# Kernel tuning notes

Measured on AMD Instinct MI355X. Metric: run time of the kernel, lower is better.

## Reference

```python
import jax, jax.numpy as jnp
import numpy as np

N = 100000
E = 1600000
IN_C, HID_C, OUT_C = 128, 128, 64


def setup_inputs() -> dict:
    key = jax.random.key(0)
    ks = jax.random.split(key, 8)
    x = jax.random.normal(ks[0], (N, IN_C), dtype=jnp.float32)
    edge_index = jax.random.randint(ks[1], (2, E), 0, N, dtype=jnp.int64)
    # Glorot-ish init for the 3 GCNConv linear weights + zero biases (PyG default)
    def glorot(k, fan_in, fan_out):
        s = jnp.sqrt(6.0 / (fan_in + fan_out))
        return jax.random.uniform(k, (fan_in, fan_out), jnp.float32, -s, s)
    return {
        "x": x,
        "edge_index": edge_index,
        "W1": glorot(ks[2], IN_C, HID_C), "b1": jnp.zeros((HID_C,), jnp.float32),
        "W2": glorot(ks[3], HID_C, HID_C), "b2": jnp.zeros((HID_C,), jnp.float32),
        "W3": glorot(ks[4], HID_C, OUT_C), "b3": jnp.zeros((OUT_C,), jnp.float32),
    }


def _gcn_norm(edge_index, num_nodes):
    # add self loops, compute D^-1/2 (A+I) D^-1/2 edge coefficients (PyG gcn_norm)
    loop = jnp.arange(num_nodes, dtype=edge_index.dtype)
    src = jnp.concatenate([edge_index[0], loop])  # [E+N]
    dst = jnp.concatenate([edge_index[1], loop])
    w = jnp.ones_like(src, dtype=jnp.float32)
    deg = jax.ops.segment_sum(w, dst, num_segments=num_nodes)
    dinv = jnp.where(deg > 0, jax.lax.rsqrt(deg), 0.0)
    norm = dinv[src] * dinv[dst]  # [E+N]
    return src, dst, norm


def _gcn_layer(x, src, dst, norm, W, b, num_nodes):
    h = x @ W                                   # [N, out]
    msg = h[src] * norm[:, None]                # gather + scale, [E+N, out]
    agg = jax.ops.segment_sum(msg, dst, num_segments=num_nodes)  # scatter-add
    return agg + b


def reference(x, edge_index, W1, b1, W2, b2, W3, b3):
    src, dst, norm = _gcn_norm(edge_index, N)
    h = jax.nn.relu(_gcn_layer(x, src, dst, norm, W1, b1, N))
    h = jax.nn.relu(_gcn_layer(h, src, dst, norm, W2, b2, N))
    h = _gcn_layer(h, src, dst, norm, W3, b3, N)
    return jax.nn.log_softmax(h, axis=-1)  # [N, OUT_C]
```

## Files before the change

### kernel.cpp

```cpp
#include <hip/hip_runtime.h>
#include <hip/hip_bf16.h>


constexpr int N_NODES = 100000;
constexpr int E_EDGES = 1600000;
constexpr int NB = (N_NODES + 127) / 128;
constexpr int BCAP = 2560;
constexpr int CHUNK = 4096;
constexpr int NCHUNK = (E_EDGES + CHUNK - 1) / CHUNK;

typedef short bf16x8 __attribute__((ext_vector_type(8)));
typedef float f32x4 __attribute__((ext_vector_type(4)));

__device__ __forceinline__ unsigned short f2bf(float f) {
    unsigned u = __float_as_uint(f);
    unsigned r = (u + 0x7fff + ((u >> 16) & 1)) >> 16;
    return (unsigned short)r;
}
__device__ __forceinline__ float bf_lo(unsigned u) { return __uint_as_float(u << 16); }
__device__ __forceinline__ float bf_hi(unsigned u) { return __uint_as_float(u & 0xffff0000u); }
__device__ __forceinline__ unsigned pack2bf(float lo, float hi) {
    return (unsigned)f2bf(lo) | ((unsigned)f2bf(hi) << 16);
}

__device__ __forceinline__ int get_idx(const void* ei, int use64, long long pos) {
    if (use64) return (int)((const long long*)ei)[pos];
    return ((const int*)ei)[pos];
}

__global__ void prep_wt_kernel(const float* __restrict__ W1, const float* __restrict__ W2,
                               const float* __restrict__ W3,
                               unsigned short* __restrict__ WT1,
                               unsigned short* __restrict__ WT2,
                               unsigned short* __restrict__ WT3,
                               const int* __restrict__ ei32, int* __restrict__ flag,
                               int* __restrict__ cursorPad) {
    const int b = blockIdx.x;
    if (b == 3) {
        for (int i = threadIdx.x; i < NB * 16; i += blockDim.x) cursorPad[i] = 0;
        if (threadIdx.x == 0) {
            int ok64 = 1;
#pragma unroll
            for (int i = 1; i < 64; i += 2) ok64 &= (ei32[i] == 0);
            *flag = ok64;
        }
        return;
    }
    const float* W = (b == 0) ? W1 : (b == 1) ? W2 : W3;
    unsigned short* WT = (b == 0) ? WT1 : (b == 1) ? WT2 : WT3;
    const int COUT = (b == 2) ? 64 : 128;
    for (int i = threadIdx.x; i < COUT * 128; i += blockDim.x) {
        int c = i >> 7;
        int k = i & 127;
        WT[c * 128 + k] = f2bf(W[k * COUT + c]);
    }
}

__global__ __launch_bounds__(256) void scatter_direct(
    const void* __restrict__ ei, const int* __restrict__ flag,
    int* __restrict__ cursorPad, unsigned* __restrict__ pairs) {
    __shared__ int h[NB];
    __shared__ int base[NB];
    __shared__ unsigned dstb[CHUNK];
    const int t = threadIdx.x;
    const int use64 = *flag;
    const int e0 = blockIdx.x * CHUNK;
    const int e1 = min(E_EDGES, e0 + CHUNK);

    for (int i = t; i < NB; i += 256) h[i] = 0;
    __syncthreads();
    for (int e = e0 + t; e < e1; e += 256) {
        unsigned d = (unsigned)get_idx(ei, use64, (long long)E_EDGES + e);
        dstb[e - e0] = d;
        atomicAdd(&h[d >> 7], 1);
    }
    __syncthreads();
    for (int i = t; i < NB; i += 256) {
        int c = h[i];
        if (c) base[i] = atomicAdd(&cursorPad[i * 16], c);
        h[i] = 0;
    }
    __syncthreads();
    for (int e = e0 + t; e < e1; e += 256) {
        unsigned s = (unsigned)get_idx(ei, use64, e);
        unsigned d = dstb[e - e0];
        int b = d >> 7;
        int r = base[b] + atomicAdd(&h[b], 1);
        if (r < BCAP) pairs[(unsigned)b * BCAP + r] = (s << 7) | (d & 127u);
    }
}

__global__ __launch_bounds__(256) void fine_sort_kernel(
    const unsigned* __restrict__ pairs, const int* __restrict__ cursorPad,
    int* __restrict__ csr, int* __restrict__ rowptr, int* __restrict__ deg,
    float* __restrict__ dinv) {
    __shared__ int h[128];
    __shared__ int rp[128];
    __shared__ int sc[128];
    const int t = threadIdx.x;
    const int b = blockIdx.x;
    const int base = b * BCAP;
    const int cnt = min(cursorPad[b * 16], BCAP);

    if (t < 128) h[t] = 0;
    __syncthreads();
    for (int i = t; i < cnt; i += 256) {
        unsigned p = pairs[base + i];
        atomicAdd(&h[p & 127u], 1);
    }
    __syncthreads();
    int v = (t < 128) ? h[t] : 0;
    if (t < 128) sc[t] = v;
    __syncthreads();
    int incl = v;
    for (int off = 1; off < 128; off <<= 1) {
        int add = (t >= off && t < 128) ? sc[t - off] : 0;
        __syncthreads();
        if (t < 128) {
            incl += add;
            sc[t] = incl;
        }
        __syncthreads();
    }
    if (t < 128) {
        rp[t] = incl - v;
        int node = b * 128 + t;
        if (node < N_NODES) {
            rowptr[node] = base + incl - v;
            deg[node] = v;
            dinv[node] = rsqrtf((float)(v + 1));
        }
        h[t] = 0;
    }
    __syncthreads();
    for (int i = t; i < cnt; i += 256) {
        unsigned p = pairs[base + i];
        int l = (int)(p & 127u);
        int r = atomicAdd(&h[l], 1);
        csr[base + rp[l] + r] = (int)(p >> 7);
    }
}

template <int COUT>
__global__ __launch_bounds__(256) void gemm_mfma_f32(const float* __restrict__ X,
                                                     const unsigned short* __restrict__ WT,
                                                     const float* __restrict__ dinv,
                                                     unsigned short* __restrict__ H) {
    constexpr int NT = COUT / 16;
    __shared__ short Albs[64 * 128];
    __shared__ short Wlds[COUT * 128];

    const int t = threadIdx.x;
    const int row0 = blockIdx.x * 64;

    for (int i = t; i < COUT * 16; i += 256) {
        int n = i >> 4, k8 = i & 15;
        bf16x8 v = *(const bf16x8*)&WT[n * 128 + k8 * 8];
        int ns = (n & ~15) | ((n & 15) ^ k8);
        *(bf16x8*)&Wlds[(k8 * COUT + ns) * 8] = v;
    }
    for (int i = t; i < 1024; i += 256) {
        int m = i >> 4, k8 = i & 15;
        int gr = min(row0 + m, N_NODES - 1);
        const float* p = &X[(size_t)gr * 128 + k8 * 8];
        float4 f0 = *(const float4*)p;
        float4 f1 = *(const float4*)(p + 4);
        bf16x8 v;
        v[0] = (short)f2bf(f0.x); v[1] = (short)f2bf(f0.y);
        v[2] = (short)f2bf(f0.z); v[3] = (short)f2bf(f0.w);
        v[4] = (short)f2bf(f1.x); v[5] = (short)f2bf(f1.y);
        v[6] = (short)f2bf(f1.z); v[7] = (short)f2bf(f1.w);
        int u = ((m >> 4) * 16 + k8) * 16 + ((m & 15) ^ k8);
        *(bf16x8*)&Albs[u * 8] = v;
    }
    __syncthreads();

    const int lane = t & 63;
    const int wv = t >> 6;
    const int l15 = lane & 15;
    const int quad = lane >> 4;

    f32x4 acc[NT];
#pragma unroll
    for (int ct = 0; ct < NT; ct++) acc[ct] = (f32x4){0.f, 0.f, 0.f, 0.f};

#pragma unroll
    for (int kcg = 0; kcg < 4; kcg++) {
        const int k8 = kcg * 4 + quad;
        bf16x8 a = *(const bf16x8*)&Albs[((wv * 16 + k8) * 16 + (l15 ^ k8)) * 8];
#pragma unroll
        for (int ct = 0; ct < NT; ct++) {
            bf16x8 b = *(const bf16x8*)&Wlds[(k8 * COUT + ct * 16 + (l15 ^ k8)) * 8];
            acc[ct] = __builtin_amdgcn_mfma_f32_16x16x32_bf16(a, b, acc[ct], 0, 0, 0);
        }
    }

    const int m0 = row0 + wv * 16;
#pragma unroll
    for (int r = 0; r < 4; r++) {
        int m = m0 + quad * 4 + r;
        if (m < N_NODES) {
            float dv = dinv[m];
#pragma unroll
            for (int ct = 0; ct < NT; ct++)
                H[(size_t)m * COUT + ct * 16 + l15] = f2bf(acc[ct][r] * dv);
        } else if (m == N_NODES) {
#pragma unroll
            for (int ct = 0; ct < NT; ct++)
                H[(size_t)m * COUT + ct * 16 + l15] = 0;
        }
    }
}

template <int COUT>
__global__ __launch_bounds__(256) void agg128_fused(
    const unsigned short* __restrict__ Hb, const int* __restrict__ rowptr,
    const int* __restrict__ deg, const int* __restrict__ csr,
    const float* __restrict__ dinv, const float* __restrict__ bias,
    const unsigned short* __restrict__ WT, unsigned short* __restrict__ Hn) {
    constexpr int NT = COUT / 16;
    constexpr int CTW = NT / 4;
    __shared__ short Wlds[COUT * 128];
    __shared__ short Atile[16 * 128];

    const int t = threadIdx.x;

    for (int i = t; i < COUT * 16; i += 256) {
        int nn = i >> 4, k8 = i & 15;
        bf16x8 v = *(const bf16x8*)&WT[nn * 128 + k8 * 8];
        int ns = (nn & ~15) | ((nn & 15) ^ k8);
        *(bf16x8*)&Wlds[(k8 * COUT + ns) * 8] = v;
    }
    if (t < 128) {
        int k8z = t >> 3, mm = 8 + (t & 7);
        *(uint4*)&Atile[(k8z * 16 + (mm ^ k8z)) * 8] = (uint4){0u, 0u, 0u, 0u};
    }

    const int lane = t & 63;
    const int wv = t >> 6;
    const int li = lane & 31;
    const int half = lane >> 5;
    const int n = blockIdx.x * 8 + wv * 2 + half;
    const unsigned li8 = (unsigned)li * 8u;
    const char* Hc = (const char*)Hb;

    uint2 s = *(const uint2*)(Hc + (size_t)n * 256u + li8);
    float a0 = bf_lo(s.x), a1 = bf_hi(s.x), a2 = bf_lo(s.y), a3 = bf_hi(s.y);

    const int start = rowptr[n];
    const int dc = deg[n];
    const int dmax = max(dc, __shfl_xor(dc, 32));

    for (int eb = 0; eb < dmax; eb += 32) {
        int myidx = N_NODES;
        if (eb + li < dc) myidx = csr[start + eb + li];
        const int jmax = min(32, dmax - eb);
        int j = 0;
        for (; j + 16 <= jmax; j += 16) {
            int idx[16];
            uint2 u[16];
#pragma unroll
            for (int q = 0; q < 16; q++) idx[q] = __shfl(myidx, j + q, 32);
#pragma unroll
            for (int q = 0; q < 16; q++)
                u[q] = *(const uint2*)(Hc + (((unsigned)idx[q] << 8) + li8));
#pragma unroll
            for (int q = 0; q < 16; q++) {
                a0 += bf_lo(u[q].x); a1 += bf_hi(u[q].x);
                a2 += bf_lo(u[q].y); a3 += bf_hi(u[q].y);
            }
        }
        for (; j + 8 <= jmax; j += 8) {
            int idx[8];
            uint2 u[8];
#pragma unroll
            for (int q = 0; q < 8; q++) idx[q] = __shfl(myidx, j + q, 32);
#pragma unroll
            for (int q = 0; q < 8; q++)
                u[q] = *(const uint2*)(Hc + (((unsigned)idx[q] << 8) + li8));
#pragma unroll
            for (int q = 0; q < 8; q++) {
                a0 += bf_lo(u[q].x); a1 += bf_hi(u[q].x);
                a2 += bf_lo(u[q].y); a3 += bf_hi(u[q].y);
            }
        }
        for (; j + 4 <= jmax; j += 4) {
            int idx[4];
            uint2 u[4];
#pragma unroll
            for (int q = 0; q < 4; q++) idx[q] = __shfl(myidx, j + q, 32);
#pragma unroll
            for (int q = 0; q < 4; q++)
                u[q] = *(const uint2*)(Hc + (((unsigned)idx[q] << 8) + li8));
#pragma unroll
            for (int q = 0; q < 4; q++) {
                a0 += bf_lo(u[q].x); a1 += bf_hi(u[q].x);
                a2 += bf_lo(u[q].y); a3 += bf_hi(u[q].y);
            }
        }
        for (; j < jmax; j++) {
            int i0 = __shfl(myidx, j, 32);
            uint2 u0 = *(const uint2*)(Hc + (((unsigned)i0 << 8) + li8));
            a0 += bf_lo(u0.x); a1 += bf_hi(u0.x);
            a2 += bf_lo(u0.y); a3 += bf_hi(u0.y);
        }
    }

    {
        const float dn = dinv[n];
        float4 bv = *(const float4*)((const char*)bias + li * 16);
        unsigned w0 = pack2bf(fmaxf(a0 * dn + bv.x, 0.f), fmaxf(a1 * dn + bv.y, 0.f));
        unsigned w1 = pack2bf(fmaxf(a2 * dn + bv.z, 0.f), fmaxf(a3 * dn + bv.w, 0.f));
        const int r = wv * 2 + half;
        const int k8 = li >> 1;
        uint2 o; o.x = w0; o.y = w1;
        *(uint2*)&Atile[(k8 * 16 + (r ^ k8)) * 8 + (li & 1) * 4] = o;
    }
    __syncthreads();

    const int l15 = lane & 15;
    const int quad = lane >> 4;
    f32x4 acc[CTW];
#pragma unroll
    for (int c = 0; c < CTW; c++) acc[c] = (f32x4){0.f, 0.f, 0.f, 0.f};

#pragma unroll
    for (int kcg = 0; kcg < 4; kcg++) {
        const int k8 = kcg * 4 + quad;
        bf16x8 a = *(const bf16x8*)&Atile[(k8 * 16 + (l15 ^ k8)) * 8];
#pragma unroll
        for (int c = 0; c < CTW; c++) {
            const int ct = wv * CTW + c;
            bf16x8 b = *(const bf16x8*)&Wlds[(k8 * COUT + ct * 16 + (l15 ^ k8)) * 8];
            acc[c] = __builtin_amdgcn_mfma_f32_16x16x32_bf16(a, b, acc[c], 0, 0, 0);
        }
    }

#pragma unroll
    for (int rr = 0; rr < 4; rr++) {
        const int row = quad * 4 + rr;
        if (row < 8) {
            const int m = blockIdx.x * 8 + row;
            const float dv = dinv[m];
#pragma unroll
            for (int c = 0; c < CTW; c++) {
                const int ct = wv * CTW + c;
                Hn[(size_t)m * COUT + ct * 16 + l15] = f2bf(acc[c][rr] * dv);
            }
        }
    }

    if (blockIdx.x == 0 && t < COUT / 4)
        *(unsigned long long*)((char*)Hn + (size_t)N_NODES * (COUT * 2) + t * 8) = 0ull;
}

__global__ __launch_bounds__(256) void aggregate64_lsm_pair(
    const unsigned short* __restrict__ Hb, const int* __restrict__ rowptr,
    const int* __restrict__ deg, const int* __restrict__ csr,
    const float* __restrict__ dinv, const float* __restrict__ bias,
    float* __restrict__ out) {
    const int lane = threadIdx.x & 63;
    const int wv = threadIdx.x >> 6;
    const int li = lane & 31;
    const int half = lane >> 5;
    const int n = blockIdx.x * 8 + wv * 2 + half;
    const unsigned li4 = (unsigned)li * 4u;
    const char* Hc = (const char*)Hb;

    unsigned s = *(const unsigned*)(Hc + (size_t)n * 128u + li4);
    float a0 = bf_lo(s), a1 = bf_hi(s);

    const int start = rowptr[n];
    const int dc = deg[n];
    const int dmax = max(dc, __shfl_xor(dc, 32));

    for (int eb = 0; eb < dmax; eb += 32) {
        int myidx = N_NODES;
        if (eb + li < dc) myidx = csr[start + eb + li];
        const int jmax = min(32, dmax - eb);
        int j = 0;
        for (; j + 16 <= jmax; j += 16) {
            int idx[16];
            unsigned u[16];
#pragma unroll
            for (int q = 0; q < 16; q++) idx[q] = __shfl(myidx, j + q, 32);
#pragma unroll
            for (int q = 0; q < 16; q++)
                u[q] = *(const unsigned*)(Hc + (((unsigned)idx[q] << 7) + li4));
#pragma unroll
            for (int q = 0; q < 16; q++) { a0 += bf_lo(u[q]); a1 += bf_hi(u[q]); }
        }
        for (; j + 8 <= jmax; j += 8) {
            int idx[8];
            unsigned u[8];
#pragma unroll
            for (int q = 0; q < 8; q++) idx[q] = __shfl(myidx, j + q, 32);
#pragma unroll
            for (int q = 0; q < 8; q++)
                u[q] = *(const unsigned*)(Hc + (((unsigned)idx[q] << 7) + li4));
#pragma unroll
            for (int q = 0; q < 8; q++) { a0 += bf_lo(u[q]); a1 += bf_hi(u[q]); }
        }
        for (; j + 4 <= jmax; j += 4) {
            int idx[4];
            unsigned u[4];
#pragma unroll
            for (int q = 0; q < 4; q++) idx[q] = __shfl(myidx, j + q, 32);
#pragma unroll
            for (int q = 0; q < 4; q++)
                u[q] = *(const unsigned*)(Hc + (((unsigned)idx[q] << 7) + li4));
#pragma unroll
            for (int q = 0; q < 4; q++) { a0 += bf_lo(u[q]); a1 += bf_hi(u[q]); }
        }
        for (; j < jmax; j++) {
            int i0 = __shfl(myidx, j, 32);
            unsigned u0 = *(const unsigned*)(Hc + (((unsigned)i0 << 7) + li4));
            a0 += bf_lo(u0); a1 += bf_hi(u0);
        }
    }

    const float dn = dinv[n];
    float2 bv = *(const float2*)((const char*)bias + li * 8);
    float v0 = a0 * dn + bv.x;
    float v1 = a1 * dn + bv.y;

    float m = fmaxf(v0, v1);
#pragma unroll
    for (int off = 16; off; off >>= 1) m = fmaxf(m, __shfl_xor(m, off));
    float e = expf(v0 - m) + expf(v1 - m);
#pragma unroll
    for (int off = 16; off; off >>= 1) e += __shfl_xor(e, off);
    float lse = m + logf(e);
    float2 o = make_float2(v0 - lse, v1 - lse);
    *(float2*)((char*)out + (size_t)n * 256 + li * 8) = o;
}

extern "C" void kernel_launch(void* const* d_in, const int* in_sizes, int n_in,
                              void* d_out, int out_size, void* d_ws, size_t ws_size,
                              hipStream_t stream) {
    const float* x = (const float*)d_in[0];
    const void* ei = d_in[1];
    const float* W1 = (const float*)d_in[2];
    const float* b1 = (const float*)d_in[3];
    const float* W2 = (const float*)d_in[4];
    const float* b2 = (const float*)d_in[5];
    const float* W3 = (const float*)d_in[6];
    const float* b3 = (const float*)d_in[7];
    float* out = (float*)d_out;

    char* w = (char*)d_ws;
    size_t off = 0;
    auto take = [&](size_t bytes) {
        char* p = w + off;
        off = (off + bytes + 255) & ~(size_t)255;
        return p;
    };
    int* flag = (int*)take(4);
    int* cursorPad = (int*)take((size_t)NB * 64);
    int* deg = (int*)take((size_t)N_NODES * 4);
    int* rowptr = (int*)take((size_t)N_NODES * 4);
    float* dinv = (float*)take((size_t)N_NODES * 4);
    int* csr = (int*)take((size_t)NB * BCAP * 4);
    unsigned short* WT1 = (unsigned short*)take(128 * 128 * 2);
    unsigned short* WT2 = (unsigned short*)take(128 * 128 * 2);
    unsigned short* WT3 = (unsigned short*)take(64 * 128 * 2);
    unsigned short* A = (unsigned short*)take((size_t)(N_NODES + 1) * 128 * 2);
    unsigned short* B = (unsigned short*)take((size_t)(N_NODES + 1) * 128 * 2);
    unsigned* pairs = (unsigned*)A;

    prep_wt_kernel<<<4, 256, 0, stream>>>(W1, W2, W3, WT1, WT2, WT3,
                                          (const int*)ei, flag, cursorPad);
    scatter_direct<<<NCHUNK, 256, 0, stream>>>(ei, flag, cursorPad, pairs);
    fine_sort_kernel<<<NB, 256, 0, stream>>>(pairs, cursorPad, csr, rowptr, deg, dinv);

    const int gg = (N_NODES + 63) / 64;
    const int g8 = N_NODES / 8;

    gemm_mfma_f32<128><<<gg, 256, 0, stream>>>(x, WT1, dinv, A);
    agg128_fused<128><<<g8, 256, 0, stream>>>(A, rowptr, deg, csr, dinv, b1, WT2, B);
    agg128_fused<64><<<g8, 256, 0, stream>>>(B, rowptr, deg, csr, dinv, b2, WT3, A);
    aggregate64_lsm_pair<<<g8, 256, 0, stream>>>(A, rowptr, deg, csr, dinv, b3, out);
}
```

Before: 378.7 us.

## Make fused aggregate+GEMM kernels persistent with per-wave node-pair MFMA

The fused aggregation+linear kernels become persistent grid-stride kernels: a fixed grid of 1024 or 2048 blocks loads the weight matrix into LDS once, and each wave then loops over node pairs. Before, 12,500 blocks each reloaded the full weight tile. Each wave now stages its own two aggregated rows in a private LDS slice and runs the full set of column MFMAs itself, so the block-wide barrier between gather and GEMM goes away. In exchange, each 16-row MFMA uses only 2 useful rows, so each wave issues about four times as many MFMAs per node as before. The load balance of the gather now depends on a static grid-stride assignment.

Result: slower. 414.9 us (+9.6%).

```diff
diff --git a/kernel.cpp b/kernel.cpp
--- a/kernel.cpp
+++ b/kernel.cpp
@@ -8,6 +8,7 @@
 constexpr int BCAP = 2560;
 constexpr int CHUNK = 4096;
 constexpr int NCHUNK = (E_EDGES + CHUNK - 1) / CHUNK;
+constexpr int NPAIR = N_NODES / 2;
 
 typedef short bf16x8 __attribute__((ext_vector_type(8)));
 typedef float f32x4 __attribute__((ext_vector_type(4)));
@@ -213,15 +214,14 @@
 }
 
 template <int COUT>
-__global__ __launch_bounds__(256) void agg128_fused(
+__global__ __launch_bounds__(256) void agg128_fused_w(
     const unsigned short* __restrict__ Hb, const int* __restrict__ rowptr,
     const int* __restrict__ deg, const int* __restrict__ csr,
     const float* __restrict__ dinv, const float* __restrict__ bias,
     const unsigned short* __restrict__ WT, unsigned short* __restrict__ Hn) {
     constexpr int NT = COUT / 16;
-    constexpr int CTW = NT / 4;
     __shared__ short Wlds[COUT * 128];
-    __shared__ short Atile[16 * 128];
+    __shared__ short Apriv[4 * 2 * 128];
 
     const int t = threadIdx.x;
 
@@ -231,127 +231,121 @@
         int ns = (nn & ~15) | ((nn & 15) ^ k8);
         *(bf16x8*)&Wlds[(k8 * COUT + ns) * 8] = v;
     }
-    if (t < 128) {
-        int k8z = t >> 3, mm = 8 + (t & 7);
-        *(uint4*)&Atile[(k8z * 16 + (mm ^ k8z)) * 8] = (uint4){0u, 0u, 0u, 0u};
-    }
+    if (blockIdx.x == 0 && t < COUT / 4)
+        *(unsigned long long*)((char*)Hn + (size_t)N_NODES * (COUT * 2) + t * 8) = 0ull;
 
     const int lane = t & 63;
     const int wv = t >> 6;
     const int li = lane & 31;
     const int half = lane >> 5;
-    const int n = blockIdx.x * 8 + wv * 2 + half;
     const unsigned li8 = (unsigned)li * 8u;
     const char* Hc = (const char*)Hb;
-
-    uint2 s = *(const uint2*)(Hc + (size_t)n * 256u + li8);
-    float a0 = bf_lo(s.x), a1 = bf_hi(s.x), a2 = bf_lo(s.y), a3 = bf_hi(s.y);
-
-    const int start = rowptr[n];
-    const int dc = deg[n];
-    const int dmax = max(dc, __shfl_xor(dc, 32));
-
-    for (int eb = 0; eb < dmax; eb += 32) {
-        int myidx = N_NODES;
-        if (eb + li < dc) myidx = csr[start + eb + li];
-        const int jmax = min(32, dmax - eb);
-        int j = 0;
-        for (; j + 16 <= jmax; j += 16) {
-            int idx[16];
-            uint2 u[16];
-#pragma unroll
-            for (int q = 0; q < 16; q++) idx[q] = __shfl(myidx, j + q, 32);
-#pragma unroll
-            for (int q = 0; q < 16; q++)
-                u[q] = *(const uint2*)(Hc + (((unsigned)idx[q] << 8) + li8));
-#pragma unroll
-            for (int q = 0; q < 16; q++) {
-                a0 += bf_lo(u[q].x); a1 += bf_hi(u[q].x);
-                a2 += bf_lo(u[q].y); a3 += bf_hi(u[q].y);
-            }
-        }
-        for (; j + 8 <= jmax; j += 8) {
-            int idx[8];
-            uint2 u[8];
-#pragma unroll
-            for (int q = 0; q < 8; q++) idx[q] = __shfl(myidx, j + q, 32);
-#pragma unroll
-            for (int q = 0; q < 8; q++)
-                u[q] = *(const uint2*)(Hc + (((unsigned)idx[q] << 8) + li8));
-#pragma unroll
-            for (int q = 0; q < 8; q++) {
-                a0 += bf_lo(u[q].x); a1 += bf_hi(u[q].x);
-                a2 += bf_lo(u[q].y); a3 += bf_hi(u[q].y);
-            }
-        }
-        for (; j + 4 <= jmax; j += 4) {
-            int idx[4];
-            uint2 u[4];
-#pragma unroll
-            for (int q = 0; q < 4; q++) idx[q] = __shfl(myidx, j + q, 32);
-#pragma unroll
-            for (int q = 0; q < 4; q++)
-                u[q] = *(const uint2*)(Hc + (((unsigned)idx[q] << 8) + li8));
-#pragma unroll
-            for (int q = 0; q < 4; q++) {
-                a0 += bf_lo(u[q].x); a1 += bf_hi(u[q].x);
-                a2 += bf_lo(u[q].y); a3 += bf_hi(u[q].y);
-            }
-        }
-        for (; j < jmax; j++) {
-            int i0 = __shfl(myidx, j, 32);
-            uint2 u0 = *(const uint2*)(Hc + (((unsigned)i0 << 8) + li8));
-            a0 += bf_lo(u0.x); a1 += bf_hi(u0.x);
-            a2 += bf_lo(u0.y); a3 += bf_hi(u0.y);
-        }
-    }
-
-    {
-        const float dn = dinv[n];
-        float4 bv = *(const float4*)((const char*)bias + li * 16);
-        unsigned w0 = pack2bf(fmaxf(a0 * dn + bv.x, 0.f), fmaxf(a1 * dn + bv.y, 0.f));
-        unsigned w1 = pack2bf(fmaxf(a2 * dn + bv.z, 0.f), fmaxf(a3 * dn + bv.w, 0.f));
-        const int r = wv * 2 + half;
-        const int k8 = li >> 1;
-        uint2 o; o.x = w0; o.y = w1;
-        *(uint2*)&Atile[(k8 * 16 + (r ^ k8)) * 8 + (li & 1) * 4] = o;
-    }
-    __syncthreads();
-
     const int l15 = lane & 15;
     const int quad = lane >> 4;
-    f32x4 acc[CTW];
-#pragma unroll
-    for (int c = 0; c < CTW; c++) acc[c] = (f32x4){0.f, 0.f, 0.f, 0.f};
-
-#pragma unroll
-    for (int kcg = 0; kcg < 4; kcg++) {
-        const int k8 = kcg * 4 + quad;
-        bf16x8 a = *(const bf16x8*)&Atile[(k8 * 16 + (l15 ^ k8)) * 8];
-#pragma unroll
-        for (int c = 0; c < CTW; c++) {
-            const int ct = wv * CTW + c;
-            bf16x8 b = *(const bf16x8*)&Wlds[(k8 * COUT + ct * 16 + (l15 ^ k8)) * 8];
-            acc[c] = __builtin_amdgcn_mfma_f32_16x16x32_bf16(a, b, acc[c], 0, 0, 0);
-        }
-    }
-
-#pragma unroll
-    for (int rr = 0; rr < 4; rr++) {
-        const int row = quad * 4 + rr;
-        if (row < 8) {
-            const int m = blockIdx.x * 8 + row;
-            const float dv = dinv[m];
-#pragma unroll
-            for (int c = 0; c < CTW; c++) {
-                const int ct = wv * CTW + c;
-                Hn[(size_t)m * COUT + ct * 16 + l15] = f2bf(acc[c][rr] * dv);
-            }
-        }
-    }
-
-    if (blockIdx.x == 0 && t < COUT / 4)
-        *(unsigned long long*)((char*)Hn + (size_t)N_NODES * (COUT * 2) + t * 8) = 0ull;
+    const int totalWaves = gridDim.x * 4;
+
+    __syncthreads();
+
+    for (int p = blockIdx.x * 4 + wv; p < NPAIR; p += totalWaves) {
+        const int n = p * 2 + half;
+
+        uint2 s = *(const uint2*)(Hc + (size_t)n * 256u + li8);
+        float a0 = bf_lo(s.x), a1 = bf_hi(s.x), a2 = bf_lo(s.y), a3 = bf_hi(s.y);
+
+        const int start = rowptr[n];
+        const int dc = deg[n];
+        const int dmax = max(dc, __shfl_xor(dc, 32));
+
+        for (int eb = 0; eb < dmax; eb += 32) {
+            int myidx = N_NODES;
+            if (eb + li < dc) myidx = csr[start + eb + li];
+            const int jmax = min(32, dmax - eb);
+            int j = 0;
+            for (; j + 16 <= jmax; j += 16) {
+                int idx[16];
+                uint2 u[16];
+#pragma unroll
+                for (int q = 0; q < 16; q++) idx[q] = __shfl(myidx, j + q, 32);
+#pragma unroll
+                for (int q = 0; q < 16; q++)
+                    u[q] = *(const uint2*)(Hc + (((unsigned)idx[q] << 8) + li8));
+#pragma unroll
+                for (int q = 0; q < 16; q++) {
+                    a0 += bf_lo(u[q].x); a1 += bf_hi(u[q].x);
+                    a2 += bf_lo(u[q].y); a3 += bf_hi(u[q].y);
+                }
+            }
+            for (; j + 8 <= jmax; j += 8) {
+                int idx[8];
+                uint2 u[8];
+#pragma unroll
+                for (int q = 0; q < 8; q++) idx[q] = __shfl(myidx, j + q, 32);
+#pragma unroll
+                for (int q = 0; q < 8; q++)
+                    u[q] = *(const uint2*)(Hc + (((unsigned)idx[q] << 8) + li8));
+#pragma unroll
+                for (int q = 0; q < 8; q++) {
+                    a0 += bf_lo(u[q].x); a1 += bf_hi(u[q].x);
+                    a2 += bf_lo(u[q].y); a3 += bf_hi(u[q].y);
+                }
+            }
+            for (; j + 4 <= jmax; j += 4) {
+                int idx[4];
+                uint2 u[4];
+#pragma unroll
+                for (int q = 0; q < 4; q++) idx[q] = __shfl(myidx, j + q, 32);
+#pragma unroll
+                for (int q = 0; q < 4; q++)
+                    u[q] = *(const uint2*)(Hc + (((unsigned)idx[q] << 8) + li8));
+#pragma unroll
+                for (int q = 0; q < 4; q++) {
+                    a0 += bf_lo(u[q].x); a1 += bf_hi(u[q].x);
+                    a2 += bf_lo(u[q].y); a3 += bf_hi(u[q].y);
+                }
+            }
+            for (; j < jmax; j++) {
+                int i0 = __shfl(myidx, j, 32);
+                uint2 u0 = *(const uint2*)(Hc + (((unsigned)i0 << 8) + li8));
+                a0 += bf_lo(u0.x); a1 += bf_hi(u0.x);
+                a2 += bf_lo(u0.y); a3 += bf_hi(u0.y);
+            }
+        }
+
+        {
+            const float dn = dinv[n];
+            float4 bv = *(const float4*)((const char*)bias + li * 16);
+            uint2 o;
+            o.x = pack2bf(fmaxf(a0 * dn + bv.x, 0.f), fmaxf(a1 * dn + bv.y, 0.f));
+            o.y = pack2bf(fmaxf(a2 * dn + bv.z, 0.f), fmaxf(a3 * dn + bv.w, 0.f));
+            *(uint2*)&Apriv[((wv * 2 + half) * 128 + li * 4)] = o;
+        }
+
+        f32x4 acc[NT];
+#pragma unroll
+        for (int c = 0; c < NT; c++) acc[c] = (f32x4){0.f, 0.f, 0.f, 0.f};
+
+#pragma unroll
+        for (int kcg = 0; kcg < 4; kcg++) {
+            const int k8 = kcg * 4 + quad;
+            bf16x8 a = *(const bf16x8*)&Apriv[(wv * 2 + (l15 & 1)) * 128 + kcg * 32 + quad * 8];
+#pragma unroll
+            for (int c = 0; c < NT; c++) {
+                bf16x8 b = *(const bf16x8*)&Wlds[(k8 * COUT + c * 16 + (l15 ^ k8)) * 8];
+                acc[c] = __builtin_amdgcn_mfma_f32_16x16x32_bf16(a, b, acc[c], 0, 0, 0);
+            }
+        }
+
+        if (quad == 0) {
+#pragma unroll
+            for (int rr = 0; rr < 2; rr++) {
+                const int m = p * 2 + rr;
+                const float dv = dinv[m];
+#pragma unroll
+                for (int c = 0; c < NT; c++)
+                    Hn[(size_t)m * COUT + c * 16 + l15] = f2bf(acc[c][rr] * dv);
+            }
+        }
+    }
 }
 
 __global__ __launch_bounds__(256) void aggregate64_lsm_pair(
@@ -477,7 +471,7 @@
     const int g8 = N_NODES / 8;
 
     gemm_mfma_f32<128><<<gg, 256, 0, stream>>>(x, WT1, dinv, A);
-    agg128_fused<128><<<g8, 256, 0, stream>>>(A, rowptr, deg, csr, dinv, b1, WT2, B);
-    agg128_fused<64><<<g8, 256, 0, stream>>>(B, rowptr, deg, csr, dinv, b2, WT3, A);
+    agg128_fused_w<128><<<1024, 256, 0, stream>>>(A, rowptr, deg, csr, dinv, b1, WT2, B);
+    agg128_fused_w<64><<<2048, 256, 0, stream>>>(B, rowptr, deg, csr, dinv, b2, WT3, A);
     aggregate64_lsm_pair<<<g8, 256, 0, stream>>>(A, rowptr, deg, csr, dinv, b3, out);
 }
```
